# Performance work log

Measured on AMD Instinct MI355X. Metric: run time of the kernel, lower is better.

The kernel has to match this reference:

```python
import jax, jax.numpy as jnp
import numpy as np

N_KNOTS = 16384
BATCH = 256
N_SAMP = 32768


def setup_inputs() -> dict:
    key = jax.random.key(0)
    k1, k2, k3 = jax.random.split(key, 3)
    # strictly increasing knot abscissae (matches module assumption of sorted x_points)
    incs = jax.random.uniform(k1, (N_KNOTS,), minval=0.01, maxval=1.0, dtype=jnp.float32)
    x_points = jnp.cumsum(incs)
    y_points = jax.random.normal(k2, (N_KNOTS,), dtype=jnp.float32)
    # samples must have a valid right bracket: x in [x_points[0], x_points[N-2])
    lo = x_points[0]
    hi = x_points[N_KNOTS - 2]
    u = jax.random.uniform(k3, (BATCH, N_SAMP), dtype=jnp.float32)
    x_samp = lo + u * (hi - lo) * 0.999
    return {"x_samp": x_samp, "x_points": x_points, "y_points": y_points}


def reference(x_samp, x_points, y_points):
    # Original: masked argmin over (x_samp - x_points) with negatives set to inf,
    # i.e. index of the largest knot <= x_samp. Equivalent to searchsorted(right)-1.
    idxi = jnp.searchsorted(x_points, x_samp, side='right') - 1  # [B, S]
    idxf = idxi + 1
    xi = x_points[idxi]  # [B, S] gather
    xf = x_points[idxf]
    yi = y_points[idxi]
    yf = y_points[idxf]
    ds = (x_samp - xi) / (xf - xi)
    return yi + ds * (yf - yi)
```

## Files before the change

kernel.cpp:

```cpp
#include <hip/hip_runtime.h>


#define NB 7936
#define NKMAX 16384

typedef float f32x4 __attribute__((ext_vector_type(4)));

__device__ __forceinline__ int bucket_of(float v, float lo, float inv_w) {
    return (int)((v - lo) * inv_w);
}

__device__ __forceinline__ unsigned pack_ys(float y, float s) {
    _Float16 hy = (_Float16)y, hs = (_Float16)s;
    unsigned short uy = __builtin_bit_cast(unsigned short, hy);
    unsigned short us = __builtin_bit_cast(unsigned short, hs);
    return (unsigned)uy | ((unsigned)us << 16);
}

__device__ __forceinline__ int hi_of_bucket(const float* xp, int nk, float lo,
                                            float inv_w, int b) {
    int loj = -1, hij = nk - 1;
    while (loj < hij) {
        int mid = (loj + hij + 1) >> 1;
        if (bucket_of(xp[mid], lo, inv_w) <= b) loj = mid; else hij = mid - 1;
    }
    if (loj < 0) loj = 0;
    if (loj > nk - 2) loj = nk - 2;
    return loj;
}

__global__ void build_tbl(const float* __restrict__ xp, const float* __restrict__ yp,
                          unsigned* __restrict__ ysg, unsigned* __restrict__ tbl,
                          int nk) {
    int i = blockIdx.x * blockDim.x + threadIdx.x;
    float lo = xp[0];
    float inv_w = (float)NB / (xp[nk - 1] - lo);
    if (i < nk) {
        float y0 = yp[i];
        float slope = 0.0f;
        if (i < nk - 1) slope = (yp[i + 1] - y0) / (xp[i + 1] - xp[i]);
        ysg[i] = pack_ys(y0, slope);
    }
    if (i < NB) {
        int hi = hi_of_bucket(xp, nk, lo, inv_w, i);
        int lo16 = (i > 0) ? hi_of_bucket(xp, nk, lo, inv_w, i - 1) : 0;
        tbl[i] = (unsigned)lo16 | ((unsigned)hi << 16);
    }
}

__global__ __launch_bounds__(1024) void interp(
        const f32x4* __restrict__ xs4, const float* __restrict__ xp,
        const unsigned* __restrict__ ysg, const unsigned* __restrict__ tbl,
        f32x4* __restrict__ out4, int n4, int nk) {
    __shared__ float sx[NKMAX];
    __shared__ unsigned sys[NKMAX];
    __shared__ unsigned sT[NB];

    const f32x4* xp4 = (const f32x4*)xp;
    f32x4* sx4 = (f32x4*)sx;
    for (int i = threadIdx.x; i < nk / 4; i += 1024) sx4[i] = xp4[i];
    const uint4* ysg4 = (const uint4*)ysg;
    uint4* sys4 = (uint4*)sys;
    for (int i = threadIdx.x; i < nk / 4; i += 1024) sys4[i] = ysg4[i];
    for (int i = threadIdx.x; i < NB; i += 1024) sT[i] = tbl[i];

    float lo = xp[0];
    float inv_w = (float)NB / (xp[nk - 1] - lo);
    __syncthreads();

    int tid = blockIdx.x * blockDim.x + threadIdx.x;
    int T = gridDim.x * blockDim.x;
    for (int t = tid; t < n4; t += 2 * T) {
        int t2 = t + T;
        bool has2 = (t2 < n4);
        f32x4 xa = __builtin_nontemporal_load(&xs4[t]);
        f32x4 xb = has2 ? __builtin_nontemporal_load(&xs4[t2]) : xa;
        float x[8] = {xa.x, xa.y, xa.z, xa.w, xb.x, xb.y, xb.z, xb.w};
        int loi[8], hii[8];
        #pragma unroll
        for (int k = 0; k < 8; k++) {
            int b = bucket_of(x[k], lo, inv_w);
            b = min(max(b, 0), NB - 1);
            unsigned p = sT[b];
            loi[k] = (int)(p & 0xffffu);
            hii[k] = (int)(p >> 16);
        }
        #pragma unroll
        for (int r = 0; r < 3; r++) {
            #pragma unroll
            for (int k = 0; k < 8; k++) {
                int mid = (loi[k] + hii[k] + 1) >> 1;
                bool ge = (sx[mid] <= x[k]);
                loi[k] = ge ? mid : loi[k];
                hii[k] = ge ? hii[k] : mid - 1;
            }
        }
        #pragma unroll
        for (int k = 0; k < 8; k++) {
            while (hii[k] > loi[k]) {
                int mid = (loi[k] + hii[k] + 1) >> 1;
                if (sx[mid] <= x[k]) loi[k] = mid; else hii[k] = mid - 1;
            }
        }
        f32x4 ra, rb;
        #pragma unroll
        for (int k = 0; k < 8; k++) {
            unsigned u = sys[loi[k]];
            float hy = (float)__builtin_bit_cast(_Float16, (unsigned short)(u & 0xffffu));
            float hs = (float)__builtin_bit_cast(_Float16, (unsigned short)(u >> 16));
            float v = fmaf(x[k] - sx[loi[k]], hs, hy);
            if (k < 4) ra[k] = v; else rb[k - 4] = v;
        }
        __builtin_nontemporal_store(ra, &out4[t]);
        if (has2) __builtin_nontemporal_store(rb, &out4[t2]);
    }
}

extern "C" void kernel_launch(void* const* d_in, const int* in_sizes, int n_in,
                              void* d_out, int out_size, void* d_ws, size_t ws_size,
                              hipStream_t stream) {
    const float* xs = (const float*)d_in[0];
    const float* xp = (const float*)d_in[1];
    const float* yp = (const float*)d_in[2];
    int ns = in_sizes[0];
    int nk = in_sizes[1];

    unsigned* ysg = (unsigned*)d_ws;
    unsigned* tbl = (unsigned*)((char*)d_ws + (size_t)nk * sizeof(unsigned));

    int na = (nk > NB ? nk : NB);
    build_tbl<<<(na + 255) / 256, 256, 0, stream>>>(xp, yp, ysg, tbl, nk);

    int n4 = ns / 4;
    interp<<<256, 1024, 0, stream>>>((const f32x4*)xs, xp, ysg, tbl,
                                     (f32x4*)d_out, n4, nk);
}
```

Before: 103.9 us.

## Replace per-bucket binary search with finer buckets and vectorized 8-wide linear scan

Raises the bucket count so each bucket holds only a few knots, stores only the bucket's starting index as a 16-bit entry, and replaces the binary search with two aligned 16-byte LDS loads of eight knots plus a branchless compare-count. A fallback loop handles buckets that extend past the window, and the selected knot value is reused so sx is not read again. The aim is to cut the dependent LDS round trips of the bisection. In exchange it adds extra compares and registers and a divergent slow path when a bucket spans more than seven knots.

Result: no change. 104.7 us (+0.8%).

```diff
diff --git a/kernel.cpp b/kernel.cpp
--- a/kernel.cpp
+++ b/kernel.cpp
@@ -1,8 +1,9 @@
 #include <hip/hip_runtime.h>
 
 
-#define NB 7936
+#define NB 14336
 #define NKMAX 16384
+#define SXPAD (NKMAX + 16)
 
 typedef float f32x4 __attribute__((ext_vector_type(4)));
 
@@ -17,20 +18,8 @@
     return (unsigned)uy | ((unsigned)us << 16);
 }
 
-__device__ __forceinline__ int hi_of_bucket(const float* xp, int nk, float lo,
-                                            float inv_w, int b) {
-    int loj = -1, hij = nk - 1;
-    while (loj < hij) {
-        int mid = (loj + hij + 1) >> 1;
-        if (bucket_of(xp[mid], lo, inv_w) <= b) loj = mid; else hij = mid - 1;
-    }
-    if (loj < 0) loj = 0;
-    if (loj > nk - 2) loj = nk - 2;
-    return loj;
-}
-
 __global__ void build_tbl(const float* __restrict__ xp, const float* __restrict__ yp,
-                          unsigned* __restrict__ ysg, unsigned* __restrict__ tbl,
+                          unsigned* __restrict__ ysg, unsigned short* __restrict__ tbl,
                           int nk) {
     int i = blockIdx.x * blockDim.x + threadIdx.x;
     float lo = xp[0];
@@ -42,32 +31,41 @@
         ysg[i] = pack_ys(y0, slope);
     }
     if (i < NB) {
-        int hi = hi_of_bucket(xp, nk, lo, inv_w, i);
-        int lo16 = (i > 0) ? hi_of_bucket(xp, nk, lo, inv_w, i - 1) : 0;
-        tbl[i] = (unsigned)lo16 | ((unsigned)hi << 16);
+        int v = 0;
+        if (i > 0) {
+            int loj = -1, hij = nk - 1;
+            while (loj < hij) {
+                int mid = (loj + hij + 1) >> 1;
+                if (bucket_of(xp[mid], lo, inv_w) <= i - 1) loj = mid; else hij = mid - 1;
+            }
+            v = loj < 0 ? 0 : (loj > nk - 2 ? nk - 2 : loj);
+        }
+        tbl[i] = (unsigned short)v;
     }
 }
 
 __global__ __launch_bounds__(1024) void interp(
         const f32x4* __restrict__ xs4, const float* __restrict__ xp,
-        const unsigned* __restrict__ ysg, const unsigned* __restrict__ tbl,
+        const unsigned* __restrict__ ysg, const unsigned short* __restrict__ tbl,
         f32x4* __restrict__ out4, int n4, int nk) {
-    __shared__ float sx[NKMAX];
+    __shared__ __align__(16) float sx[SXPAD];
     __shared__ unsigned sys[NKMAX];
-    __shared__ unsigned sT[NB];
+    __shared__ unsigned short sT[NB];
 
     const f32x4* xp4 = (const f32x4*)xp;
-    f32x4* sx4 = (f32x4*)sx;
-    for (int i = threadIdx.x; i < nk / 4; i += 1024) sx4[i] = xp4[i];
+    f32x4* sx4w = (f32x4*)sx;
+    for (int i = threadIdx.x; i < nk / 4; i += 1024) sx4w[i] = xp4[i];
     const uint4* ysg4 = (const uint4*)ysg;
     uint4* sys4 = (uint4*)sys;
     for (int i = threadIdx.x; i < nk / 4; i += 1024) sys4[i] = ysg4[i];
     for (int i = threadIdx.x; i < NB; i += 1024) sT[i] = tbl[i];
+    if (threadIdx.x < SXPAD - NKMAX) sx[NKMAX + threadIdx.x] = __builtin_inff();
 
     float lo = xp[0];
     float inv_w = (float)NB / (xp[nk - 1] - lo);
     __syncthreads();
 
+    const f32x4* sx4 = (const f32x4*)sx;
     int tid = blockIdx.x * blockDim.x + threadIdx.x;
     int T = gridDim.x * blockDim.x;
     for (int t = tid; t < n4; t += 2 * T) {
@@ -76,39 +74,51 @@
         f32x4 xa = __builtin_nontemporal_load(&xs4[t]);
         f32x4 xb = has2 ? __builtin_nontemporal_load(&xs4[t2]) : xa;
         float x[8] = {xa.x, xa.y, xa.z, xa.w, xb.x, xb.y, xb.z, xb.w};
-        int loi[8], hii[8];
+
+        int al[8];
+        f32x4 w0[8], w1[8];
         #pragma unroll
         for (int k = 0; k < 8; k++) {
             int b = bucket_of(x[k], lo, inv_w);
             b = min(max(b, 0), NB - 1);
-            unsigned p = sT[b];
-            loi[k] = (int)(p & 0xffffu);
-            hii[k] = (int)(p >> 16);
+            int l = sT[b];
+            al[k] = l & ~3;
+            int q = al[k] >> 2;
+            w0[k] = sx4[q];
+            w1[k] = sx4[q + 1];
         }
+
+        int j[8];
+        float xi[8];
         #pragma unroll
-        for (int r = 0; r < 3; r++) {
-            #pragma unroll
-            for (int k = 0; k < 8; k++) {
-                int mid = (loi[k] + hii[k] + 1) >> 1;
-                bool ge = (sx[mid] <= x[k]);
-                loi[k] = ge ? mid : loi[k];
-                hii[k] = ge ? hii[k] : mid - 1;
+        for (int k = 0; k < 8; k++) {
+            float c0 = w0[k].x, c1 = w0[k].y, c2 = w0[k].z, c3 = w0[k].w;
+            float c4 = w1[k].x, c5 = w1[k].y, c6 = w1[k].z, c7 = w1[k].w;
+            float xk = x[k];
+            int cnt = (c1 <= xk) + (c2 <= xk) + (c3 <= xk) + (c4 <= xk)
+                    + (c5 <= xk) + (c6 <= xk) + (c7 <= xk);
+            float v = c0;
+            v = (c1 <= xk) ? c1 : v;
+            v = (c2 <= xk) ? c2 : v;
+            v = (c3 <= xk) ? c3 : v;
+            v = (c4 <= xk) ? c4 : v;
+            v = (c5 <= xk) ? c5 : v;
+            v = (c6 <= xk) ? c6 : v;
+            v = (c7 <= xk) ? c7 : v;
+            j[k] = al[k] + cnt;
+            xi[k] = v;
+            if (cnt == 7) {
+                while (sx[j[k] + 1] <= xk) { j[k]++; xi[k] = sx[j[k]]; }
             }
         }
-        #pragma unroll
-        for (int k = 0; k < 8; k++) {
-            while (hii[k] > loi[k]) {
-                int mid = (loi[k] + hii[k] + 1) >> 1;
-                if (sx[mid] <= x[k]) loi[k] = mid; else hii[k] = mid - 1;
-            }
-        }
+
         f32x4 ra, rb;
         #pragma unroll
         for (int k = 0; k < 8; k++) {
-            unsigned u = sys[loi[k]];
+            unsigned u = sys[j[k]];
             float hy = (float)__builtin_bit_cast(_Float16, (unsigned short)(u & 0xffffu));
             float hs = (float)__builtin_bit_cast(_Float16, (unsigned short)(u >> 16));
-            float v = fmaf(x[k] - sx[loi[k]], hs, hy);
+            float v = fmaf(x[k] - xi[k], hs, hy);
             if (k < 4) ra[k] = v; else rb[k - 4] = v;
         }
         __builtin_nontemporal_store(ra, &out4[t]);
@@ -126,7 +136,7 @@
     int nk = in_sizes[1];
 
     unsigned* ysg = (unsigned*)d_ws;
-    unsigned* tbl = (unsigned*)((char*)d_ws + (size_t)nk * sizeof(unsigned));
+    unsigned short* tbl = (unsigned short*)((char*)d_ws + (size_t)nk * sizeof(unsigned));
 
     int na = (nk > NB ? nk : NB);
     build_tbl<<<(na + 255) / 256, 256, 0, stream>>>(xp, yp, ysg, tbl, nk);
```
